# Kernel tuning notes

Hardware: AMD Instinct MI355X
Metric: run time of the kernel (lower is better)

Reference implementation:

```python
import jax, jax.numpy as jnp
import numpy as np

B, S, D, H = 2, 2048, 768, 12
DK = D // H
NEG = -1000000000.0


def setup_inputs() -> dict:
    key = jax.random.key(0)
    ks = jax.random.split(key, 12)
    inp = {
        "query": jax.random.normal(ks[0], (B, S, D), jnp.float32),
        "key": jax.random.normal(ks[1], (B, S, D), jnp.float32),
        "value": jax.random.normal(ks[2], (B, S, D), jnp.float32),
        "mask": jax.random.randint(ks[3], (B, 1, 1, S), 0, 2, jnp.int32),
    }
    sc = 1.0 / np.sqrt(D)
    inp["Wq"] = jax.random.normal(ks[4], (D, D), jnp.float32) * sc
    inp["bq"] = jnp.zeros((D,), jnp.float32)
    inp["Wk"] = jax.random.normal(ks[5], (D, D), jnp.float32) * sc
    inp["bk"] = jnp.zeros((D,), jnp.float32)
    inp["Wv"] = jax.random.normal(ks[6], (D, D), jnp.float32) * sc
    inp["bv"] = jnp.zeros((D,), jnp.float32)
    inp["Wo"] = jax.random.normal(ks[7], (D, D), jnp.float32) * sc
    inp["bo"] = jnp.zeros((D,), jnp.float32)
    return inp


def reference(query, key, value, mask, Wq, bq, Wk, bk, Wv, bv, Wo, bo):
    b = query.shape[0]
    # QKV projections -> [B, H, S, DK]
    def proj(x, W, bias):
        y = jnp.einsum('bsd,de->bse', x, W.T) + bias
        return y.reshape(b, -1, H, DK).transpose(0, 2, 1, 3)
    q = proj(query, Wq, bq)
    k = proj(key, Wk, bk)
    v = proj(value, Wv, bv)
    # scores: [B, H, S, S]
    scores = jnp.einsum('bhqd,bhkd->bhqk', q, k) / jnp.sqrt(jnp.float32(DK))
    scores = jnp.where(mask == 0, jnp.float32(NEG), scores)
    p = jax.nn.softmax(scores, axis=-1)
    x = jnp.einsum('bhqk,bhkd->bhqd', p, v)  # [B, H, S, DK]
    x = x.transpose(0, 2, 1, 3).reshape(b, -1, H * DK)
    return jnp.einsum('bsd,de->bse', x, Wo.T) + bo
```

## Files before the change

kernel.cpp:

```cpp
#include <hip/hip_runtime.h>

typedef unsigned short u16;
typedef __attribute__((ext_vector_type(8))) __bf16 bf16x8;
typedef __attribute__((ext_vector_type(8))) short s16x8;
typedef __attribute__((ext_vector_type(8))) unsigned short u16x8;
typedef __attribute__((ext_vector_type(4))) float f32x4;
typedef __attribute__((ext_vector_type(4))) unsigned short u16x4;
typedef __attribute__((ext_vector_type(4))) float fl4;
typedef __attribute__((ext_vector_type(4))) int i32x4;

#define MFMA(a, b, c) __builtin_amdgcn_mfma_f32_16x16x32_bf16((a), (b), (c), 0, 0, 0)
#define QSC 0.18033688011112042f

__device__ __forceinline__ u16 f2bf(float f) {
  __bf16 h = (__bf16)f;
  return __builtin_bit_cast(unsigned short, h);
}

__device__ __forceinline__ float bf2f(u16 u) {
  union { unsigned u; float f; } v; v.u = ((unsigned)u) << 16;
  return v.f;
}

__device__ __forceinline__ void gll16(const u16* g, u16* l) {
  typedef __attribute__((address_space(1))) unsigned int gu32;
  typedef __attribute__((address_space(3))) unsigned int lu32;
  __builtin_amdgcn_global_load_lds((gu32*)g, (lu32*)l, 16, 0, 0);
}


__global__ __launch_bounds__(256) void k_convert_w(
    const float* __restrict__ Wq, const float* __restrict__ Wk,
    const float* __restrict__ Wv, const float* __restrict__ Wo,
    u16* __restrict__ wqkv, u16* __restrict__ wob) {
  const int n = 3072 * 192;
  for (int i = blockIdx.x * 256 + threadIdx.x; i < n; i += gridDim.x * 256) {
    int row = i / 192;
    int col = (i - row * 192) * 4;
    const float* src; u16* dst; float sc = 1.0f;
    if (row < 768)       { src = Wq + row * 768;          dst = wqkv + row * 768; sc = QSC; }
    else if (row < 1536) { src = Wk + (row - 768) * 768;  dst = wqkv + row * 768; }
    else if (row < 2304) { src = Wv + (row - 1536) * 768; dst = wqkv + row * 768; }
    else                 { src = Wo + (row - 2304) * 768; dst = wob + (row - 2304) * 768; }
    fl4 f = *(const fl4*)(src + col);
    u16x4 o;
    o[0] = f2bf(f[0] * sc); o[1] = f2bf(f[1] * sc);
    o[2] = f2bf(f[2] * sc); o[3] = f2bf(f[3] * sc);
    *(u16x4*)(dst + col) = o;
  }
}


__global__ __launch_bounds__(256) void k_gemm_qkv(
    const float* __restrict__ xq, const float* __restrict__ xk,
    const float* __restrict__ xv, const u16* __restrict__ wqkv,
    const float* __restrict__ bq, const float* __restrict__ bk_,
    const float* __restrict__ bv_,
    u16* __restrict__ Qb, u16* __restrict__ Kb, u16* __restrict__ Vtb) {
  __shared__ __align__(16) u16 Abuf[2][128 * 32];
  __shared__ __align__(16) u16 Bbuf[2][128 * 32];
  const int tid = threadIdx.x;
  const int bid = blockIdx.x;
  const int wid = (bid & 7) * 72 + (bid >> 3);
  const int row0 = (wid / 18) * 128, col0 = (wid % 18) * 128;
  const int seg = col0 / 768;
  const float* A32 = (seg == 0) ? xq : ((seg == 1) ? xk : xv);
  const int w = tid >> 6, lane = tid & 63, lr = lane & 15, kg = lane >> 4;
  const int wr = (w >> 1) * 64, wc = (w & 1) * 64;

  const int c0 = tid, c1 = tid + 256;
  const int r0c = c0 >> 2, g0 = (c0 & 3) ^ ((r0c >> 1) & 3);
  const int r1c = c1 >> 2, g1 = (c1 & 3) ^ ((r1c >> 1) & 3);
  const float* aS0 = A32 + (size_t)(row0 + r0c) * 768 + g0 * 8;
  const float* aS1 = A32 + (size_t)(row0 + r1c) * 768 + g1 * 8;
  const u16* bS0 = wqkv + (size_t)(col0 + r0c) * 768 + g0 * 8;
  const u16* bS1 = wqkv + (size_t)(col0 + r1c) * 768 + g1 * 8;

  f32x4 acc[4][4];
  f32x4 zero = {0.f, 0.f, 0.f, 0.f};
#pragma unroll
  for (int i = 0; i < 4; i++)
#pragma unroll
    for (int j = 0; j < 4; j++) acc[i][j] = zero;

  int aoff[4], boff[4];
#pragma unroll
  for (int mi = 0; mi < 4; mi++) {
    int r = wr + mi * 16 + lr;
    aoff[mi] = r * 32 + (kg ^ ((r >> 1) & 3)) * 8;
  }
#pragma unroll
  for (int ni = 0; ni < 4; ni++) {
    int r = wc + ni * 16 + lr;
    boff[ni] = r * 32 + (kg ^ ((r >> 1) & 3)) * 8;
  }

  fl4 ar[4];
#define LOADA(kt) { ar[0] = *(const fl4*)(aS0 + (kt) * 32);       \
                    ar[1] = *(const fl4*)(aS0 + (kt) * 32 + 4);   \
                    ar[2] = *(const fl4*)(aS1 + (kt) * 32);       \
                    ar[3] = *(const fl4*)(aS1 + (kt) * 32 + 4); }
#define WRITEA(buf) { u16x8 t0, t1;                               \
    t0[0]=f2bf(ar[0][0]); t0[1]=f2bf(ar[0][1]); t0[2]=f2bf(ar[0][2]); t0[3]=f2bf(ar[0][3]); \
    t0[4]=f2bf(ar[1][0]); t0[5]=f2bf(ar[1][1]); t0[6]=f2bf(ar[1][2]); t0[7]=f2bf(ar[1][3]); \
    t1[0]=f2bf(ar[2][0]); t1[1]=f2bf(ar[2][1]); t1[2]=f2bf(ar[2][2]); t1[3]=f2bf(ar[2][3]); \
    t1[4]=f2bf(ar[3][0]); t1[5]=f2bf(ar[3][1]); t1[6]=f2bf(ar[3][2]); t1[7]=f2bf(ar[3][3]); \
    *(u16x8*)((buf) + c0 * 8) = t0; *(u16x8*)((buf) + c1 * 8) = t1; }
#define STAGEB(kt, buf) { gll16(bS0 + (kt) * 32, (buf) + c0 * 8); \
                          gll16(bS1 + (kt) * 32, (buf) + c1 * 8); }

  LOADA(0);
  STAGEB(0, Bbuf[0]);
  WRITEA(Abuf[0]);
  __syncthreads();

  for (int kt = 0; kt < 24; kt++) {
    const int cur = kt & 1;
    if (kt < 23) { LOADA(kt + 1); STAGEB(kt + 1, Bbuf[cur ^ 1]); }
    bf16x8 af[4], bfr[4];
#pragma unroll
    for (int mi = 0; mi < 4; mi++) af[mi] = *(const bf16x8*)(Abuf[cur] + aoff[mi]);
#pragma unroll
    for (int ni = 0; ni < 4; ni++) bfr[ni] = *(const bf16x8*)(Bbuf[cur] + boff[ni]);
#pragma unroll
    for (int mi = 0; mi < 4; mi++)
#pragma unroll
      for (int ni = 0; ni < 4; ni++)
        acc[mi][ni] = MFMA(af[mi], bfr[ni], acc[mi][ni]);
    __syncthreads();
    if (kt < 23) {
      WRITEA(Abuf[cur ^ 1]);
      __syncthreads();
    }
  }
#undef LOADA
#undef WRITEA
#undef STAGEB

  const float* bias = (seg == 0) ? bq : ((seg == 1) ? bk_ : bv_);
  const float bsc = (seg == 0) ? QSC : 1.0f;
  const int ncol0 = col0 - seg * 768;
#pragma unroll
  for (int ni = 0; ni < 4; ni++) {
    const int n = ncol0 + wc + ni * 16 + lr;
    const float bval = bias[n] * bsc;
    const int hh = n >> 6, dk = n & 63;
#pragma unroll
    for (int mi = 0; mi < 4; mi++)
#pragma unroll
      for (int j = 0; j < 4; j++) {
        const int m = row0 + wr + mi * 16 + kg * 4 + j;
        const int bb = m >> 11, ss = m & 2047;
        const u16 val = f2bf(acc[mi][ni][j] + bval);
        if (seg == 0)
          Qb[((size_t)((bb * 12 + hh) * 2048 + ss)) * 64 + dk] = val;
        else if (seg == 1)
          Kb[((size_t)((bb * 12 + hh) * 2048 + ss)) * 64 + dk] = val;
        else
          Vtb[((size_t)((bb * 12 + hh) * 64 + dk)) * 2048 + ss] = val;
      }
  }
}


__global__ __launch_bounds__(256) void k_attn(
    const u16* __restrict__ Qb, const u16* __restrict__ Kb,
    const u16* __restrict__ Vtb, const int* __restrict__ mask,
    u16* __restrict__ o_part, float* __restrict__ l_part) {
  __shared__ __align__(16) u16 Ks[2][64 * 64];
  __shared__ __align__(16) u16 Vs[2][64 * 64];
  __shared__ __align__(16) u16 Ps[4][32 * 64];
  __shared__ __align__(16) int mlds[1024];
  const int bid = blockIdx.x;
  const int wid = (bid & 7) * 96 + (bid >> 3);
  const int qt = wid & 15;
  const int gh = wid >> 4;
  const int bh = gh >> 1, half = gh & 1;
  const int b = bh / 12;
  const int kvb = half << 10;
  const int tid = threadIdx.x, w = tid >> 6, lane = tid & 63;
  const int lr = lane & 15, g = lane >> 4;
  const int q0 = qt * 128 + w * 32;
  const u16* Qh = Qb + (size_t)bh * (2048 * 64);
  const u16* Kh = Kb + (size_t)bh * (2048 * 64);
  const u16* Vh = Vtb + (size_t)bh * (64 * 2048);
  const int* mb = mask + b * 2048;
  u16* Pw = Ps[w];

  *(i32x4*)(mlds + tid * 4) = *(const i32x4*)(mb + kvb + tid * 4);

  bf16x8 aq[2][2];
#pragma unroll
  for (int mi = 0; mi < 2; mi++)
#pragma unroll
    for (int ks = 0; ks < 2; ks++)
      aq[mi][ks] = *(const bf16x8*)(Qh + (q0 + mi * 16 + lr) * 64 + ks * 32 + g * 8);

  f32x4 zero = {0.f, 0.f, 0.f, 0.f};
  f32x4 o[2][4];
#pragma unroll
  for (int mi = 0; mi < 2; mi++)
#pragma unroll
    for (int di = 0; di < 4; di++) o[mi][di] = zero;
  f32x4 o_l[2];
  o_l[0] = zero; o_l[1] = zero;

  s16x8 ov = {0x3F80, 0x3F80, 0x3F80, 0x3F80, 0x3F80, 0x3F80, 0x3F80, 0x3F80};
  bf16x8 ones = __builtin_bit_cast(bf16x8, ov);

  const int c0 = tid, c1 = tid + 256;
  const int sr0 = c0 >> 3, sg0 = (c0 & 7) ^ (sr0 & 7);
  const int sr1 = c1 >> 3, sg1 = (c1 & 7) ^ (sr1 & 7);
  const u16* kA0 = Kh + (size_t)kvb * 64 + sr0 * 64 + sg0 * 8;
  const u16* kA1 = Kh + (size_t)kvb * 64 + sr1 * 64 + sg1 * 8;
  const u16* vA0 = Vh + sr0 * 2048 + kvb + sg0 * 8;
  const u16* vA1 = Vh + sr1 * 2048 + kvb + sg1 * 8;

#define STAGE(u) { u16* kd = Ks[(u)&1]; u16* vd = Vs[(u)&1];           \
    gll16(kA0 + (u) * 4096, kd + c0 * 8);                              \
    gll16(kA1 + (u) * 4096, kd + c1 * 8);                              \
    gll16(vA0 + (u) * 64,  vd + c0 * 8);                               \
    gll16(vA1 + (u) * 64,  vd + c1 * 8); }

  STAGE(0);
  __syncthreads();

  for (int t = 0; t < 16; t++) {
    if (t < 15) STAGE(t + 1);
    const u16* Kc = Ks[t & 1];
    const u16* Vc = Vs[t & 1];

    f32x4 s[2][4];
#pragma unroll
    for (int ni = 0; ni < 4; ni++) {
      const int row = ni * 16 + lr;
      bf16x8 b0 = *(const bf16x8*)(Kc + row * 64 + ((g ^ (row & 7)) << 3));
      bf16x8 b1 = *(const bf16x8*)(Kc + row * 64 + (((4 + g) ^ (row & 7)) << 3));
#pragma unroll
      for (int mi = 0; mi < 2; mi++) {
        f32x4 z = MFMA(b0, aq[mi][0], zero);
        z = MFMA(b1, aq[mi][1], z);
        s[mi][ni] = z;
      }
    }
#pragma unroll
    for (int ni = 0; ni < 4; ni++) {
      const i32x4 mk4 = *(const i32x4*)(mlds + t * 64 + ni * 16 + g * 4);
#pragma unroll
      for (int mi = 0; mi < 2; mi++)
#pragma unroll
        for (int j = 0; j < 4; j++)
          s[mi][ni][j] = mk4[j] ? s[mi][ni][j] : -1e9f;
    }

#pragma unroll
    for (int mi = 0; mi < 2; mi++) {
      const int prow = mi * 16 + lr;
      const int rbase = prow * 128, sw = (prow & 7) << 4;
#pragma unroll
      for (int ni = 0; ni < 4; ni++) {
        u16x4 pk;
#pragma unroll
        for (int j = 0; j < 4; j++)
          pk[j] = f2bf(__builtin_amdgcn_exp2f(s[mi][ni][j]));
        *(u16x4*)(Pw + ((rbase + ((ni * 32 + g * 8) ^ sw)) >> 1)) = pk;
      }
    }

#pragma unroll
    for (int ks2 = 0; ks2 < 2; ks2++) {
      bf16x8 ap[2];
#pragma unroll
      for (int mi = 0; mi < 2; mi++) {
        const int prow = mi * 16 + lr;
        const int byt = prow * 128 + ((ks2 * 64 + g * 16) ^ ((prow & 7) << 4));
        ap[mi] = *(const bf16x8*)(Pw + (byt >> 1));
      }
#pragma unroll
      for (int di = 0; di < 4; di++) {
        const int vrow = di * 16 + lr;
        bf16x8 bv = *(const bf16x8*)(Vc + vrow * 64 + (((ks2 * 4 + g) ^ (vrow & 7)) << 3));
#pragma unroll
        for (int mi = 0; mi < 2; mi++)
          o[mi][di] = MFMA(ap[mi], bv, o[mi][di]);
      }
#pragma unroll
      for (int mi = 0; mi < 2; mi++)
        o_l[mi] = MFMA(ap[mi], ones, o_l[mi]);
    }

    if (t < 15) __syncthreads();
  }
#undef STAGE

  u16* opw = o_part + (size_t)(half * 24 + bh) * (2048 * 64);
  float* lpw = l_part + (size_t)(half * 24 + bh) * 2048;
#pragma unroll
  for (int mi = 0; mi < 2; mi++) {
#pragma unroll
    for (int di = 0; di < 4; di++)
#pragma unroll
      for (int j = 0; j < 4; j++) {
        const int row = q0 + mi * 16 + g * 4 + j;
        opw[(size_t)row * 64 + di * 16 + lr] = f2bf(o[mi][di][j]);
      }
    if (lr == 0) {
#pragma unroll
      for (int j = 0; j < 4; j++)
        lpw[q0 + mi * 16 + g * 4 + j] = o_l[mi][j];
    }
  }
}


__global__ __launch_bounds__(256) void k_combine(
    const u16* __restrict__ o_part, const float* __restrict__ l_part,
    u16* __restrict__ attn) {
  const int idx = blockIdx.x * 256 + threadIdx.x;
  const int row = idx >> 3;
  const int c8 = (idx & 7) << 3;
  const size_t HALF_O = (size_t)24 * 2048 * 64;
  u16x8 a0 = *(const u16x8*)(o_part + (size_t)row * 64 + c8);
  u16x8 a1 = *(const u16x8*)(o_part + HALF_O + (size_t)row * 64 + c8);
  const float l = l_part[row] + l_part[24 * 2048 + row];
  const float rcp = 1.0f / l;
  u16x8 r;
#pragma unroll
  for (int j = 0; j < 8; j++)
    r[j] = f2bf((bf2f(a0[j]) + bf2f(a1[j])) * rcp);
  const int bh = row >> 11, s = row & 2047;
  const int b = bh / 12, h = bh - b * 12;
  *(u16x8*)(attn + (size_t)(b * 2048 + s) * 768 + h * 64 + c8) = r;
}


__global__ __launch_bounds__(256) void k_gemm_out(
    const u16* __restrict__ attn, const u16* __restrict__ wob,
    const float* __restrict__ bo, float* __restrict__ out) {
  __shared__ __align__(16) u16 As[2][128 * 32];
  __shared__ __align__(16) u16 Bs[2][128 * 32];
  const int tid = threadIdx.x;
  const int bid = blockIdx.x;
  const int wid = (bid & 7) * 24 + (bid >> 3);
  const int row0 = (wid / 6) * 128, col0 = (wid % 6) * 128;
  const int w = tid >> 6, lane = tid & 63, lr = lane & 15, kg = lane >> 4;
  const int wr = (w >> 1) * 64, wc = (w & 1) * 64;

  const int c0 = tid, c1 = tid + 256;
  const int r0c = c0 >> 2, g0 = (c0 & 3) ^ ((r0c >> 1) & 3);
  const int r1c = c1 >> 2, g1 = (c1 & 3) ^ ((r1c >> 1) & 3);
  const u16* aS0 = attn + (size_t)(row0 + r0c) * 768 + g0 * 8;
  const u16* aS1 = attn + (size_t)(row0 + r1c) * 768 + g1 * 8;
  const u16* bS0 = wob + (size_t)(col0 + r0c) * 768 + g0 * 8;
  const u16* bS1 = wob + (size_t)(col0 + r1c) * 768 + g1 * 8;

  f32x4 acc[4][4];
  f32x4 zero = {0.f, 0.f, 0.f, 0.f};
#pragma unroll
  for (int i = 0; i < 4; i++)
#pragma unroll
    for (int j = 0; j < 4; j++) acc[i][j] = zero;

  int aoff[4], boff[4];
#pragma unroll
  for (int mi = 0; mi < 4; mi++) {
    int r = wr + mi * 16 + lr;
    aoff[mi] = r * 32 + (kg ^ ((r >> 1) & 3)) * 8;
  }
#pragma unroll
  for (int ni = 0; ni < 4; ni++) {
    int r = wc + ni * 16 + lr;
    boff[ni] = r * 32 + (kg ^ ((r >> 1) & 3)) * 8;
  }

#define STAGE(kt) { u16* ad = As[(kt)&1]; u16* bd = Bs[(kt)&1];   \
    gll16(aS0 + (kt) * 32, ad + c0 * 8);                          \
    gll16(aS1 + (kt) * 32, ad + c1 * 8);                          \
    gll16(bS0 + (kt) * 32, bd + c0 * 8);                          \
    gll16(bS1 + (kt) * 32, bd + c1 * 8); }

  STAGE(0);
  __syncthreads();

  for (int kt = 0; kt < 24; kt++) {
    const int cur = kt & 1;
    if (kt < 23) STAGE(kt + 1);
    bf16x8 af[4], bfr[4];
#pragma unroll
    for (int mi = 0; mi < 4; mi++) af[mi] = *(const bf16x8*)(As[cur] + aoff[mi]);
#pragma unroll
    for (int ni = 0; ni < 4; ni++) bfr[ni] = *(const bf16x8*)(Bs[cur] + boff[ni]);
#pragma unroll
    for (int mi = 0; mi < 4; mi++)
#pragma unroll
      for (int ni = 0; ni < 4; ni++)
        acc[mi][ni] = MFMA(af[mi], bfr[ni], acc[mi][ni]);
    if (kt < 23) __syncthreads();
  }
#undef STAGE

#pragma unroll
  for (int ni = 0; ni < 4; ni++) {
    const int n = col0 + wc + ni * 16 + lr;
    const float bval = bo[n];
#pragma unroll
    for (int mi = 0; mi < 4; mi++)
#pragma unroll
      for (int j = 0; j < 4; j++) {
        const int m = row0 + wr + mi * 16 + kg * 4 + j;
        out[(size_t)m * 768 + n] = acc[mi][ni][j] + bval;
      }
  }
}


extern "C" void kernel_launch(void* const* d_in, const int* in_sizes, int n_in,
                              void* d_out, int out_size, void* d_ws, size_t ws_size,
                              hipStream_t stream) {
  const float* q = (const float*)d_in[0];
  const float* k = (const float*)d_in[1];
  const float* v = (const float*)d_in[2];
  const int* mask = (const int*)d_in[3];
  const float* Wq = (const float*)d_in[4];
  const float* bq = (const float*)d_in[5];
  const float* Wk = (const float*)d_in[6];
  const float* bk = (const float*)d_in[7];
  const float* Wv = (const float*)d_in[8];
  const float* bv = (const float*)d_in[9];
  const float* Wo = (const float*)d_in[10];
  const float* bo = (const float*)d_in[11];
  float* out = (float*)d_out;

  u16* scratch = (u16*)d_ws;
  u16* wqkv = scratch + (size_t)3 * 4096 * 768;
  u16* wob = wqkv + (size_t)2304 * 768;
  u16* Qb = wob + (size_t)768 * 768;
  u16* Kb = Qb + (size_t)4096 * 768;
  u16* Vtb = Kb + (size_t)4096 * 768;
  u16* attn = Vtb + (size_t)4096 * 768;

  u16* o_part = scratch;
  float* l_part = (float*)(scratch + (size_t)2 * 24 * 2048 * 64);

  k_convert_w<<<dim3(2304), dim3(256), 0, stream>>>(Wq, Wk, Wv, Wo, wqkv, wob);
  k_gemm_qkv<<<dim3(576), dim3(256), 0, stream>>>(q, k, v, wqkv, bq, bk, bv, Qb, Kb, Vtb);
  k_attn<<<dim3(768), dim3(256), 0, stream>>>(Qb, Kb, Vtb, mask, o_part, l_part);
  k_combine<<<dim3(1536), dim3(256), 0, stream>>>(o_part, l_part, attn);
  k_gemm_out<<<dim3(192), dim3(256), 0, stream>>>(attn, wob, bo, out);
}
```

Before: 112.6 us.

## Pre-convert activations to bf16 and stage both GEMM operands via direct LDS loads

Adds a separate kernel that converts the fp32 query/key/value activations to bf16 in workspace. The QKV GEMM then loads both A and B tiles with global_load_lds straight into shared memory, which removes the register round-trip, the in-loop conversion and one barrier per k-step. The cost is an extra kernel launch plus writing and re-reading 18.9 MB of bf16 activations, against the fp32 A tiles that each block previously read directly.

```diff
diff --git a/kernel.cpp b/kernel.cpp
--- a/kernel.cpp
+++ b/kernel.cpp
@@ -26,6 +26,23 @@
   typedef __attribute__((address_space(1))) unsigned int gu32;
   typedef __attribute__((address_space(3))) unsigned int lu32;
   __builtin_amdgcn_global_load_lds((gu32*)g, (lu32*)l, 16, 0, 0);
+}
+
+
+__global__ __launch_bounds__(256) void k_convert_x(
+    const float* __restrict__ q, const float* __restrict__ k,
+    const float* __restrict__ v, u16* __restrict__ xb) {
+  const int NG = 4096 * 768 / 4;
+  const int n = 3 * NG;
+  for (int i = blockIdx.x * 256 + threadIdx.x; i < n; i += gridDim.x * 256) {
+    int seg = i / NG;
+    int j = (i - seg * NG) * 4;
+    const float* s = (seg == 0) ? q : ((seg == 1) ? k : v);
+    fl4 f = *(const fl4*)(s + j);
+    u16x4 o;
+    o[0] = f2bf(f[0]); o[1] = f2bf(f[1]); o[2] = f2bf(f[2]); o[3] = f2bf(f[3]);
+    *(u16x4*)(xb + seg * (4096 * 768) + j) = o;
+  }
 }
 
 
@@ -52,8 +69,7 @@
 
 
 __global__ __launch_bounds__(256) void k_gemm_qkv(
-    const float* __restrict__ xq, const float* __restrict__ xk,
-    const float* __restrict__ xv, const u16* __restrict__ wqkv,
+    const u16* __restrict__ xb, const u16* __restrict__ wqkv,
     const float* __restrict__ bq, const float* __restrict__ bk_,
     const float* __restrict__ bv_,
     u16* __restrict__ Qb, u16* __restrict__ Kb, u16* __restrict__ Vtb) {
@@ -64,15 +80,15 @@
   const int wid = (bid & 7) * 72 + (bid >> 3);
   const int row0 = (wid / 18) * 128, col0 = (wid % 18) * 128;
   const int seg = col0 / 768;
-  const float* A32 = (seg == 0) ? xq : ((seg == 1) ? xk : xv);
+  const u16* A = xb + (size_t)seg * (4096 * 768);
   const int w = tid >> 6, lane = tid & 63, lr = lane & 15, kg = lane >> 4;
   const int wr = (w >> 1) * 64, wc = (w & 1) * 64;
 
   const int c0 = tid, c1 = tid + 256;
   const int r0c = c0 >> 2, g0 = (c0 & 3) ^ ((r0c >> 1) & 3);
   const int r1c = c1 >> 2, g1 = (c1 & 3) ^ ((r1c >> 1) & 3);
-  const float* aS0 = A32 + (size_t)(row0 + r0c) * 768 + g0 * 8;
-  const float* aS1 = A32 + (size_t)(row0 + r1c) * 768 + g1 * 8;
+  const u16* aS0 = A + (size_t)(row0 + r0c) * 768 + g0 * 8;
+  const u16* aS1 = A + (size_t)(row0 + r1c) * 768 + g1 * 8;
   const u16* bS0 = wqkv + (size_t)(col0 + r0c) * 768 + g0 * 8;
   const u16* bS1 = wqkv + (size_t)(col0 + r1c) * 768 + g1 * 8;
 
@@ -95,28 +111,18 @@
     boff[ni] = r * 32 + (kg ^ ((r >> 1) & 3)) * 8;
   }
 
-  fl4 ar[4];
-#define LOADA(kt) { ar[0] = *(const fl4*)(aS0 + (kt) * 32);       \
-                    ar[1] = *(const fl4*)(aS0 + (kt) * 32 + 4);   \
-                    ar[2] = *(const fl4*)(aS1 + (kt) * 32);       \
-                    ar[3] = *(const fl4*)(aS1 + (kt) * 32 + 4); }
-#define WRITEA(buf) { u16x8 t0, t1;                               \
-    t0[0]=f2bf(ar[0][0]); t0[1]=f2bf(ar[0][1]); t0[2]=f2bf(ar[0][2]); t0[3]=f2bf(ar[0][3]); \
-    t0[4]=f2bf(ar[1][0]); t0[5]=f2bf(ar[1][1]); t0[6]=f2bf(ar[1][2]); t0[7]=f2bf(ar[1][3]); \
-    t1[0]=f2bf(ar[2][0]); t1[1]=f2bf(ar[2][1]); t1[2]=f2bf(ar[2][2]); t1[3]=f2bf(ar[2][3]); \
-    t1[4]=f2bf(ar[3][0]); t1[5]=f2bf(ar[3][1]); t1[6]=f2bf(ar[3][2]); t1[7]=f2bf(ar[3][3]); \
-    *(u16x8*)((buf) + c0 * 8) = t0; *(u16x8*)((buf) + c1 * 8) = t1; }
-#define STAGEB(kt, buf) { gll16(bS0 + (kt) * 32, (buf) + c0 * 8); \
-                          gll16(bS1 + (kt) * 32, (buf) + c1 * 8); }
-
-  LOADA(0);
-  STAGEB(0, Bbuf[0]);
-  WRITEA(Abuf[0]);
+#define STAGE(kt) { u16* ad = Abuf[(kt)&1]; u16* bd = Bbuf[(kt)&1];   \
+    gll16(aS0 + (kt) * 32, ad + c0 * 8);                              \
+    gll16(aS1 + (kt) * 32, ad + c1 * 8);                              \
+    gll16(bS0 + (kt) * 32, bd + c0 * 8);                              \
+    gll16(bS1 + (kt) * 32, bd + c1 * 8); }
+
+  STAGE(0);
   __syncthreads();
 
   for (int kt = 0; kt < 24; kt++) {
     const int cur = kt & 1;
-    if (kt < 23) { LOADA(kt + 1); STAGEB(kt + 1, Bbuf[cur ^ 1]); }
+    if (kt < 23) STAGE(kt + 1);
     bf16x8 af[4], bfr[4];
 #pragma unroll
     for (int mi = 0; mi < 4; mi++) af[mi] = *(const bf16x8*)(Abuf[cur] + aoff[mi]);
@@ -127,15 +133,9 @@
 #pragma unroll
       for (int ni = 0; ni < 4; ni++)
         acc[mi][ni] = MFMA(af[mi], bfr[ni], acc[mi][ni]);
-    __syncthreads();
-    if (kt < 23) {
-      WRITEA(Abuf[cur ^ 1]);
-      __syncthreads();
-    }
-  }
-#undef LOADA
-#undef WRITEA
-#undef STAGEB
+    if (kt < 23) __syncthreads();
+  }
+#undef STAGE
 
   const float* bias = (seg == 0) ? bq : ((seg == 1) ? bk_ : bv_);
   const float bsc = (seg == 0) ? QSC : 1.0f;
@@ -431,19 +431,20 @@
   const float* bo = (const float*)d_in[11];
   float* out = (float*)d_out;
 
-  u16* scratch = (u16*)d_ws;
-  u16* wqkv = scratch + (size_t)3 * 4096 * 768;
+  u16* xb = (u16*)d_ws;
+  u16* wqkv = xb + (size_t)3 * 4096 * 768;
   u16* wob = wqkv + (size_t)2304 * 768;
   u16* Qb = wob + (size_t)768 * 768;
   u16* Kb = Qb + (size_t)4096 * 768;
   u16* Vtb = Kb + (size_t)4096 * 768;
   u16* attn = Vtb + (size_t)4096 * 768;
 
-  u16* o_part = scratch;
-  float* l_part = (float*)(scratch + (size_t)2 * 24 * 2048 * 64);
-
+  u16* o_part = xb;
+  float* l_part = (float*)(xb + (size_t)2 * 24 * 2048 * 64);
+
+  k_convert_x<<<dim3(4608), dim3(256), 0, stream>>>(q, k, v, xb);
   k_convert_w<<<dim3(2304), dim3(256), 0, stream>>>(Wq, Wk, Wv, Wo, wqkv, wob);
-  k_gemm_qkv<<<dim3(576), dim3(256), 0, stream>>>(q, k, v, wqkv, bq, bk, bv, Qb, Kb, Vtb);
+  k_gemm_qkv<<<dim3(576), dim3(256), 0, stream>>>(xb, wqkv, bq, bk, bv, Qb, Kb, Vtb);
   k_attn<<<dim3(768), dim3(256), 0, stream>>>(Qb, Kb, Vtb, mask, o_part, l_part);
   k_combine<<<dim3(1536), dim3(256), 0, stream>>>(o_part, l_part, attn);
   k_gemm_out<<<dim3(192), dim3(256), 0, stream>>>(attn, wob, bo, out);
```

Result: slower. 119.1 us (+5.8%).
